# Performance work log

Hardware: AMD Instinct MI355X
Metric: run time of the kernel (lower is better)

The kernel has to match this reference:

```python
import jax, jax.numpy as jnp
import numpy as np

NFFT = 512
HOP = 256
N_FREQ = NFFT // 2


def _imdct_kernels():
    # Matches _get_imdct_kernels: windowed IMDCT cosine basis, shape [nfft, nfft//2]
    def kernel_fn(time, freq):
        win = np.sin(np.pi * (2 * time + 1) / (2.0 * NFFT))
        return np.cos(np.pi / NFFT * (2 * time + 1 + NFFT / 2.0) * (freq + 0.5)) * win
    k = np.fromfunction(kernel_fn, (NFFT, N_FREQ), dtype=np.float64)
    return jnp.asarray(k.astype(np.float32))  # [nfft, n_freq]


def setup_inputs() -> dict:
    key = jax.random.key(0)
    spec = jax.random.normal(key, (16, 1, N_FREQ, 4096), dtype=jnp.float32)
    return {"spec": spec, "kernels": _imdct_kernels()}


def reference(spec, kernels):
    # spec: [B, 1, n_freq, T]; kernels: [nfft, n_freq]
    B, _, _, T = spec.shape
    # conv2d with (n_freq,1) kernel == per-frame basis matmul over frequency
    frames = jnp.einsum('bft,kf->btk', spec[:, 0], kernels) * (4.0 / NFFT)  # [B, T, nfft]
    # conv_transpose2d with identity-diagonal kernel and stride=hop == overlap-add
    L = (T - 1) * HOP + NFFT
    idx = jnp.arange(T)[:, None] * HOP + jnp.arange(NFFT)[None, :]  # [T, nfft]
    out = jnp.zeros((B, L), dtype=spec.dtype).at[:, idx].add(frames)
    return out
```

## Files before the change

### kernel.cpp

```cpp
#include <hip/hip_runtime.h>
#include <stdint.h>

#define NFREQ 256
#define NB 16
#define NT 4096
#define LOUT 1048832
#define BK 64
#define AROW_U32 36
#define BGRP_B 1040

typedef __bf16 bf16;
typedef __bf16 bf16x8 __attribute__((ext_vector_type(8)));
typedef float floatx4 __attribute__((ext_vector_type(4)));

__device__ inline uint32_t f_as_u(float x) { union { float f; uint32_t u; } v; v.f = x; return v.u; }

__global__ __launch_bounds__(256) void build_kb(const float* __restrict__ ker,
                                                bf16* __restrict__ kb) {
    int idx = blockIdx.x * 256 + threadIdx.x;
    int r = idx >> 9, f = idx & 511;
    float v = (f < 256) ? ker[(r + 256) * 256 + f] : ker[r * 256 + (f - 256)];
    uint32_t u = f_as_u(v * 0.0078125f);
    uint32_t rr = (u + 0x7fffu + ((u >> 16) & 1u)) >> 16;
    union { uint16_t u; bf16 b; } o; o.u = (uint16_t)rr;
    kb[idx] = o.b;
}

__device__ inline void load_lds16(const bf16* g, void* l) {
    __builtin_amdgcn_global_load_lds((const __attribute__((address_space(1))) uint32_t*)g,
                                     (__attribute__((address_space(3))) uint32_t*)l,
                                     16, 0, 0);
}

__global__ __launch_bounds__(256, 2) void imdct_gemm(const float* __restrict__ spec,
                                                     const bf16* __restrict__ kb,
                                                     float* __restrict__ out) {
    __shared__ uint32_t As[128 * AROW_U32];
    __shared__ uint8_t  Bs[32 * BGRP_B];

    const int jt = blockIdx.x;
    const int b  = blockIdx.y;
    const int tid = threadIdx.x;
    const int lane = tid & 63;
    const int w = tid >> 6;
    const int wm = w >> 1, wn = w & 1;
    const int j0 = jt * 128;

    const int q2 = tid & 3;
    const int p  = (tid >> 2) & 31;
    const int h  = tid >> 7;

    const int row = lane & 15, q = lane >> 4;

    const float* specb = spec + (size_t)b * NFREQ * NT;

    floatx4 acc[4][8] = {};

    for (int kki = 0; kki < 8; ++kki) {
        const int kk = kki * BK;
        const int fbase = kk & 255;
        const int tbase = j0 - (kk < 256 ? 1 : 0);
        const bool edge = (tbase < 0) | (tbase > NT - 128);
        const float* r0 = specb + (size_t)(fbase + 2 * p) * NT;
        const float* r1 = r0 + NT;

        for (int i = 0; i < 4; ++i) {
            const int c = q2 + 16 * h + 4 * i;
            const int t0 = tbase + c * 4;
            float v0[4], v1[4];
            if (!edge) {
                float4 a4 = *reinterpret_cast<const float4*>(r0 + t0);
                float4 b4 = *reinterpret_cast<const float4*>(r1 + t0);
                v0[0] = a4.x; v0[1] = a4.y; v0[2] = a4.z; v0[3] = a4.w;
                v1[0] = b4.x; v1[1] = b4.y; v1[2] = b4.z; v1[3] = b4.w;
            } else {
                for (int e = 0; e < 4; ++e) {
                    int t = t0 + e;
                    bool ok = (unsigned)t < (unsigned)NT;
                    v0[e] = ok ? r0[t] : 0.0f;
                    v1[e] = ok ? r1[t] : 0.0f;
                }
            }
            for (int e = 0; e < 4; ++e) {
                uint32_t pk = ((f_as_u(v0[e]) + 0x8000u) >> 16) |
                              ((f_as_u(v1[e]) + 0x8000u) & 0xffff0000u);
                As[(c * 4 + e) * AROW_U32 + p] = pk;
            }
        }

        for (int g = 0; g < 8; ++g) {
            int grp = w * 8 + g;
            const bf16* gsrc = kb + (size_t)(grp * 8 + (lane >> 3)) * 512 + kk + (lane & 7) * 8;
            load_lds16(gsrc, Bs + grp * BGRP_B);
        }
        __syncthreads();

        for (int ks = 0; ks < 2; ++ks) {
            bf16x8 af[4], bfr[8];
            for (int i = 0; i < 4; ++i)
                af[i] = *reinterpret_cast<const bf16x8*>(
                    (const uint8_t*)As + (wm * 64 + i * 16 + row) * 144 + ks * 64 + q * 16);
            for (int jn = 0; jn < 8; ++jn) {
                int n = wn * 128 + jn * 16 + row;
                bfr[jn] = *reinterpret_cast<const bf16x8*>(
                    Bs + (n >> 3) * BGRP_B + (n & 7) * 128 + ks * 64 + q * 16);
            }
            for (int i = 0; i < 4; ++i)
                for (int jn = 0; jn < 8; ++jn)
                    acc[i][jn] = __builtin_amdgcn_mfma_f32_16x16x32_bf16(af[i], bfr[jn], acc[i][jn], 0, 0, 0);
        }
        __syncthreads();
    }

    for (int i = 0; i < 4; ++i) {
        int jb = j0 + wm * 64 + i * 16 + q * 4;
        for (int e = 0; e < 4; ++e) {
            int j = jb + e;
            if (j <= 4096) {
                float* orow = out + (size_t)b * LOUT + (size_t)j * 256;
                for (int jn = 0; jn < 8; ++jn)
                    orow[wn * 128 + jn * 16 + row] = acc[i][jn][e];
            }
        }
    }
}

extern "C" void kernel_launch(void* const* d_in, const int* in_sizes, int n_in,
                              void* d_out, int out_size, void* d_ws, size_t ws_size,
                              hipStream_t stream) {
    const float* spec = (const float*)d_in[0];
    const float* ker  = (const float*)d_in[1];
    float* out = (float*)d_out;

    bf16* kb = (bf16*)d_ws;

    build_kb<<<512, 256, 0, stream>>>(ker, kb);
    imdct_gemm<<<dim3(33, NB), 256, 0, stream>>>(spec, kb, out);
}
```

Before: 149.3 us.

## Stage transposed spectrum tile once in LDS and shrink M tile to 64

The spectrum tile for a 65-frame window is loaded once into LDS as a transposed bf16 array and reused across both K halves through a one-row offset, instead of being reloaded each K step. The M tile drops from 128 to 64 output frames, giving 65x16 blocks instead of 33x16, with each wave covering 64 output columns. Spectrum loads are now scalar, strided per frequency with shuffle-based packing rather than float4, and rounding changes to round-to-nearest-even. Occupancy and CU fill should improve, at the cost of less B-tile reuse per block and possibly less coalesced global reads.

```diff
diff --git a/kernel.cpp b/kernel.cpp
--- a/kernel.cpp
+++ b/kernel.cpp
@@ -5,23 +5,26 @@
 #define NB 16
 #define NT 4096
 #define LOUT 1048832
-#define BK 64
-#define AROW_U32 36
-#define BGRP_B 1040
+#define TROWS 65
+#define TROW 132
+#define BGRP 1088
 
 typedef __bf16 bf16;
 typedef __bf16 bf16x8 __attribute__((ext_vector_type(8)));
 typedef float floatx4 __attribute__((ext_vector_type(4)));
 
 __device__ inline uint32_t f_as_u(float x) { union { float f; uint32_t u; } v; v.f = x; return v.u; }
+__device__ inline uint32_t bf16r(float x) {
+    uint32_t u = f_as_u(x);
+    return (u + 0x7fffu + ((u >> 16) & 1u)) >> 16;
+}
 
 __global__ __launch_bounds__(256) void build_kb(const float* __restrict__ ker,
                                                 bf16* __restrict__ kb) {
     int idx = blockIdx.x * 256 + threadIdx.x;
     int r = idx >> 9, f = idx & 511;
     float v = (f < 256) ? ker[(r + 256) * 256 + f] : ker[r * 256 + (f - 256)];
-    uint32_t u = f_as_u(v * 0.0078125f);
-    uint32_t rr = (u + 0x7fffu + ((u >> 16) & 1u)) >> 16;
+    uint32_t rr = bf16r(v * 0.0078125f);
     union { uint16_t u; bf16 b; } o; o.u = (uint16_t)rr;
     kb[idx] = o.b;
 }
@@ -35,91 +38,95 @@
 __global__ __launch_bounds__(256, 2) void imdct_gemm(const float* __restrict__ spec,
                                                      const bf16* __restrict__ kb,
                                                      float* __restrict__ out) {
-    __shared__ uint32_t As[128 * AROW_U32];
-    __shared__ uint8_t  Bs[32 * BGRP_B];
+    __shared__ uint32_t Tt[TROWS * TROW];
+    __shared__ uint8_t  Bs[32 * BGRP];
 
     const int jt = blockIdx.x;
     const int b  = blockIdx.y;
-    const int tid = threadIdx.x;
-    const int lane = tid & 63;
-    const int w = tid >> 6;
-    const int wm = w >> 1, wn = w & 1;
-    const int j0 = jt * 128;
+    const int tid = threadIdx.x, lane = tid & 63, w = tid >> 6;
+    const int j0 = jt * 64;
+    const float* sb = spec + (size_t)b * NFREQ * NT;
 
-    const int q2 = tid & 3;
-    const int p  = (tid >> 2) & 31;
-    const int h  = tid >> 7;
+    {
+        const int lpar = lane & 1, lt = lane >> 1;
+        const int fpw = w * 32;
+        for (int rb = 0; rb < 4; ++rb) {
+            float v[16];
+            #pragma unroll
+            for (int i = 0; i < 16; ++i) {
+                int r = rb * 16 + i;
+                int tc = r >> 5, fpi = r & 31;
+                int f = (fpw + fpi) * 2 + lpar;
+                int t = j0 - 1 + tc * 32 + lt;
+                v[i] = ((unsigned)t < (unsigned)NT) ? sb[(size_t)f * NT + t] : 0.0f;
+            }
+            #pragma unroll
+            for (int i = 0; i < 16; i += 2) {
+                int r = rb * 16 + i;
+                int tc = r >> 5, fpi = r & 31;
+                int tl = tc * 32 + lt;
+                uint32_t h0 = bf16r(v[i]);     uint32_t o0 = (uint32_t)__shfl_xor((int)h0, 1);
+                uint32_t h1 = bf16r(v[i + 1]); uint32_t o1 = (uint32_t)__shfl_xor((int)h1, 1);
+                if (lpar == 0) {
+                    uint2 pk; pk.x = (h0 & 0xffffu) | (o0 << 16); pk.y = (h1 & 0xffffu) | (o1 << 16);
+                    *reinterpret_cast<uint2*>(&Tt[tl * TROW + fpw + fpi]) = pk;
+                }
+            }
+        }
+        int f = w * 64 + lane;
+        int t = j0 + 63;
+        float v = ((unsigned)t < (unsigned)NT) ? sb[(size_t)f * NT + t] : 0.0f;
+        uint32_t h = bf16r(v); uint32_t o = (uint32_t)__shfl_xor((int)h, 1);
+        if (lpar == 0) Tt[64 * TROW + w * 32 + lt] = (h & 0xffffu) | (o << 16);
+    }
 
-    const int row = lane & 15, q = lane >> 4;
-
-    const float* specb = spec + (size_t)b * NFREQ * NT;
-
-    floatx4 acc[4][8] = {};
+    const int row16 = lane & 15, q = lane >> 4;
+    floatx4 acc[4][4] = {};
+    const uint8_t* Tb = reinterpret_cast<const uint8_t*>(Tt);
 
     for (int kki = 0; kki < 8; ++kki) {
-        const int kk = kki * BK;
-        const int fbase = kk & 255;
-        const int tbase = j0 - (kk < 256 ? 1 : 0);
-        const bool edge = (tbase < 0) | (tbase > NT - 128);
-        const float* r0 = specb + (size_t)(fbase + 2 * p) * NT;
-        const float* r1 = r0 + NT;
-
-        for (int i = 0; i < 4; ++i) {
-            const int c = q2 + 16 * h + 4 * i;
-            const int t0 = tbase + c * 4;
-            float v0[4], v1[4];
-            if (!edge) {
-                float4 a4 = *reinterpret_cast<const float4*>(r0 + t0);
-                float4 b4 = *reinterpret_cast<const float4*>(r1 + t0);
-                v0[0] = a4.x; v0[1] = a4.y; v0[2] = a4.z; v0[3] = a4.w;
-                v1[0] = b4.x; v1[1] = b4.y; v1[2] = b4.z; v1[3] = b4.w;
-            } else {
-                for (int e = 0; e < 4; ++e) {
-                    int t = t0 + e;
-                    bool ok = (unsigned)t < (unsigned)NT;
-                    v0[e] = ok ? r0[t] : 0.0f;
-                    v1[e] = ok ? r1[t] : 0.0f;
-                }
-            }
-            for (int e = 0; e < 4; ++e) {
-                uint32_t pk = ((f_as_u(v0[e]) + 0x8000u) >> 16) |
-                              ((f_as_u(v1[e]) + 0x8000u) & 0xffff0000u);
-                As[(c * 4 + e) * AROW_U32 + p] = pk;
-            }
-        }
-
-        for (int g = 0; g < 8; ++g) {
-            int grp = w * 8 + g;
-            const bf16* gsrc = kb + (size_t)(grp * 8 + (lane >> 3)) * 512 + kk + (lane & 7) * 8;
-            load_lds16(gsrc, Bs + grp * BGRP_B);
+        #pragma unroll
+        for (int g8 = 0; g8 < 8; ++g8) {
+            int g = w * 8 + g8;
+            const bf16* gsrc = kb + (size_t)(g * 8 + (lane >> 3)) * 512 + kki * 64 + (lane & 7) * 8;
+            load_lds16(gsrc, Bs + g * BGRP);
         }
         __syncthreads();
 
+        const int toff = (kki >= 4) ? 1 : 0;
+        const int kbyte = (kki & 3) * 128;
+        #pragma unroll
         for (int ks = 0; ks < 2; ++ks) {
-            bf16x8 af[4], bfr[8];
+            bf16x8 af[4], bfr[4];
+            #pragma unroll
             for (int i = 0; i < 4; ++i)
                 af[i] = *reinterpret_cast<const bf16x8*>(
-                    (const uint8_t*)As + (wm * 64 + i * 16 + row) * 144 + ks * 64 + q * 16);
-            for (int jn = 0; jn < 8; ++jn) {
-                int n = wn * 128 + jn * 16 + row;
+                    Tb + (size_t)(i * 16 + row16 + toff) * 528 + kbyte + ks * 64 + q * 16);
+            #pragma unroll
+            for (int jn = 0; jn < 4; ++jn) {
+                int n = w * 64 + jn * 16 + row16;
                 bfr[jn] = *reinterpret_cast<const bf16x8*>(
-                    Bs + (n >> 3) * BGRP_B + (n & 7) * 128 + ks * 64 + q * 16);
+                    Bs + (n >> 3) * BGRP + (n & 7) * 128 + ks * 64 + q * 16);
             }
+            #pragma unroll
             for (int i = 0; i < 4; ++i)
-                for (int jn = 0; jn < 8; ++jn)
+                #pragma unroll
+                for (int jn = 0; jn < 4; ++jn)
                     acc[i][jn] = __builtin_amdgcn_mfma_f32_16x16x32_bf16(af[i], bfr[jn], acc[i][jn], 0, 0, 0);
         }
         __syncthreads();
     }
 
+    #pragma unroll
     for (int i = 0; i < 4; ++i) {
-        int jb = j0 + wm * 64 + i * 16 + q * 4;
+        #pragma unroll
         for (int e = 0; e < 4; ++e) {
-            int j = jb + e;
+            int j = j0 + i * 16 + q * 4 + e;
             if (j <= 4096) {
-                float* orow = out + (size_t)b * LOUT + (size_t)j * 256;
-                for (int jn = 0; jn < 8; ++jn)
-                    orow[wn * 128 + jn * 16 + row] = acc[i][jn][e];
+                float* orow = out + (size_t)b * LOUT + (size_t)j * 256 + w * 64;
+                #pragma unroll
+                for (int jn = 0; jn < 4; ++jn)
+                    orow[jn * 16 + row16] = acc[i][jn][e];
             }
         }
     }
@@ -135,5 +142,5 @@
     bf16* kb = (bf16*)d_ws;
 
     build_kb<<<512, 256, 0, stream>>>(ker, kb);
-    imdct_gemm<<<dim3(33, NB), 256, 0, stream>>>(spec, kb, out);
+    imdct_gemm<<<dim3(65, NB), 256, 0, stream>>>(spec, kb, out);
 }
```

New measurement: 145.6 us. 1.03x faster.
